# Kernel optimization log

Measured on AMD Instinct MI355X. Metric: run time of the kernel, lower is better.

## Reference

```python
import jax, jax.numpy as jnp
import numpy as np

HQ, HKV, HD = 16, 4, 64  # q heads, kv heads, head dim
ROPE_BASE = 10000.0


def _rope_tables(n, dim):
    inv_freq = 1.0 / (ROPE_BASE ** (jnp.arange(0, dim, 2, dtype=jnp.float32) / dim))
    t = jnp.arange(n, dtype=jnp.float32)
    freqs = jnp.outer(t, inv_freq)           # [N, dim/2]
    emb = jnp.concatenate([freqs, freqs], -1)  # [N, dim]
    return jnp.cos(emb), jnp.sin(emb)


def _rotate_half(x):
    h = x.shape[-1] // 2
    return jnp.concatenate([-x[..., h:], x[..., :h]], axis=-1)


def _apply_rope(x, cos, sin):
    # x: [B, N, H, D]; cos/sin: [N, D]
    c = cos[None, :, None, :]
    s = sin[None, :, None, :]
    return x * c + _rotate_half(x) * s


def setup_inputs() -> dict:
    key = jax.random.key(0)
    ks = jax.random.split(key, 5)
    B, N, D = 2, 4096, 1024
    kvD = HKV * HD
    sc = 0.02
    return {
        "x": jax.random.normal(ks[0], (B, N, D), jnp.float32),
        "Wq": jax.random.normal(ks[1], (D, D), jnp.float32) * sc,
        "Wk": jax.random.normal(ks[2], (D, kvD), jnp.float32) * sc,
        "Wv": jax.random.normal(ks[3], (D, kvD), jnp.float32) * sc,
        "Wo": jax.random.normal(ks[4], (D, D), jnp.float32) * sc,
    }


def reference(x, Wq, Wk, Wv, Wo):
    B, N, D = x.shape
    G = HQ // HKV
    Q = (x @ Wq).reshape(B, N, HQ, HD)
    K = (x @ Wk).reshape(B, N, HKV, HD)
    V = (x @ Wv).reshape(B, N, HKV, HD)

    cos, sin = _rope_tables(N, HD)
    Q = _apply_rope(Q, cos, sin)
    K = _apply_rope(K, cos, sin)

    # GQA: expand KV heads to match Q heads (repeat_interleave over head dim)
    K = jnp.repeat(K, G, axis=2)  # [B, N, HQ, HD]
    V = jnp.repeat(V, G, axis=2)

    Q = Q.transpose(0, 2, 1, 3)  # [B, HQ, N, HD]
    K = K.transpose(0, 2, 1, 3)
    V = V.transpose(0, 2, 1, 3)

    scores = jnp.einsum('bhqd,bhkd->bhqk', Q, K) / jnp.sqrt(jnp.float32(HD))
    attn = jax.nn.softmax(scores, axis=-1)
    out = jnp.einsum('bhqk,bhkd->bhqd', attn, V)  # [B, HQ, N, HD]
    out = out.transpose(0, 2, 1, 3).reshape(B, N, D)
    return out @ Wo
```

## Files before the change

kernel.cpp:

```cpp
#include <hip/hip_runtime.h>

#define HQn   16
#define HKVn  4
#define HDn   64
#define SEQN  4096
#define NB    2
#define DM    1024
#define KVD   256
#define NPACK 1536

#define QSCALE 0.18033688011112042f

typedef __attribute__((ext_vector_type(8))) short short8;
typedef __attribute__((ext_vector_type(4))) float f32x4;

#define MFMA16 __builtin_amdgcn_mfma_f32_16x16x32_bf16
#define EXP2F(x) __builtin_amdgcn_exp2f(x)

static __device__ __forceinline__ unsigned short f2bf(float f){
  union { float f; unsigned int u; } c; c.f = f;
  unsigned int r = c.u + 0x7fffu + ((c.u >> 16) & 1u);
  return (unsigned short)(r >> 16);
}

#if __has_builtin(__builtin_amdgcn_cvt_pk_bf16_f32)
typedef __attribute__((ext_vector_type(2))) __bf16 bf16x2v;
static __device__ __forceinline__ unsigned int pk_bf2(float a, float b){
  union { bf16x2v v; unsigned int u; } c;
  c.v = __builtin_amdgcn_cvt_pk_bf16_f32(a, b);
  return c.u;
}
#else
static __device__ __forceinline__ unsigned int pk_bf2(float a, float b){
  union { float f; unsigned int u; } ca, cb; ca.f = a; cb.f = b;
  return ((ca.u + 0x8000u) >> 16) | ((cb.u + 0x8000u) & 0xFFFF0000u);
}
#endif

static __device__ __forceinline__ void gl2lds16(const void* g, void* l){
  __builtin_amdgcn_global_load_lds(
      (const __attribute__((address_space(1))) void*)g,
      (__attribute__((address_space(3))) void*)l, 16, 0, 0);
}

__global__ __launch_bounds__(256) void prep_k(
    const float* __restrict__ x,
    const float* __restrict__ Wq, const float* __restrict__ Wk,
    const float* __restrict__ Wv, const float* __restrict__ Wo,
    float* __restrict__ ct, float* __restrict__ st,
    unsigned short* __restrict__ xb,
    unsigned short* __restrict__ Wqkv_t, unsigned short* __restrict__ Wot)
{
  const int id = blockIdx.x, tid = threadIdx.x;
  __shared__ float tile[64][65];

  if (id < 1024) {
    int idx = id * 256 + tid;
    int t = idx >> 6, d = idx & 63;
    int i = d & 31;
    float inv = 1.0f / powf(10000.0f, (float)i * (1.0f/32.0f));
    float ang = (float)t * inv;
    ct[t*HDn + d] = cosf(ang);
    st[t*HDn + d] = sinf(ang);
    return;
  }

  if (id < 5120) {
    size_t i = ((size_t)(id - 1024) * 256 + tid) * 8;
    float4 a = *(const float4*)(x + i);
    float4 b = *(const float4*)(x + i + 4);
    short8 o;
    o[0]=f2bf(a.x); o[1]=f2bf(a.y); o[2]=f2bf(a.z); o[3]=f2bf(a.w);
    o[4]=f2bf(b.x); o[5]=f2bf(b.y); o[6]=f2bf(b.z); o[7]=f2bf(b.w);
    *(short8*)(xb + i) = o;
    return;
  }

  const int cid = id - 5120;
  const int z = cid & 3;
  const int by = (cid >> 2) & 15;
  const int bx = cid >> 6;

  const float* W; unsigned short* D; int srcN, nOff;
  if      (z == 0) { W = Wq; D = Wqkv_t; srcN = DM;  nOff = 0;    }
  else if (z == 1) { W = Wo; D = Wot;    srcN = DM;  nOff = 0;    }
  else if (z == 2) { W = Wk; D = Wqkv_t; srcN = KVD; nOff = 1024; }
  else             { W = Wv; D = Wqkv_t; srcN = KVD; nOff = 1280; }
  const int n0 = by * 64;
  if (n0 >= srcN) return;
  const int k0 = bx * 64;

  const int lr = tid >> 4, lc = (tid & 15) * 4;
  #pragma unroll
  for (int p = 0; p < 4; p++) {
    float4 v = *(const float4*)&W[(size_t)(k0 + lr + p*16) * srcN + n0 + lc];
    tile[lr + p*16][lc+0] = v.x; tile[lr + p*16][lc+1] = v.y;
    tile[lr + p*16][lc+2] = v.z; tile[lr + p*16][lc+3] = v.w;
  }
  __syncthreads();

  const int nn = tid >> 2, kc = (tid & 3) * 16;
  unsigned short* dp = D + (size_t)(nOff + n0 + nn) * DM + k0 + kc;
  #pragma unroll
  for (int q = 0; q < 4; q++) {
    ushort4 o;
    o.x = f2bf(tile[kc + q*4 + 0][nn]);
    o.y = f2bf(tile[kc + q*4 + 1][nn]);
    o.z = f2bf(tile[kc + q*4 + 2][nn]);
    o.w = f2bf(tile[kc + q*4 + 3][nn]);
    *(ushort4*)(dp + q*4) = o;
  }
}

__global__ __launch_bounds__(256) void qkv2_k(
    const unsigned short* __restrict__ A, const unsigned short* __restrict__ Bt,
    const float* __restrict__ ct, const float* __restrict__ st,
    unsigned short* __restrict__ Qo, unsigned short* __restrict__ Ko,
    unsigned short* __restrict__ Vo)
{
  __shared__ __align__(16) short As[2][128][32];
  __shared__ __align__(16) short Bs[2][128][32];

  const int m0 = blockIdx.x * 128, n0 = blockIdx.y * 128;
  const int tid = threadIdx.x, lane = tid & 63, w = tid >> 6;
  const int wm = w >> 1, wn = w & 1;
  const int ln = lane & 15, quad = lane >> 4;

  f32x4 acc[4][4];
  #pragma unroll
  for (int i = 0; i < 4; i++)
    #pragma unroll
    for (int j = 0; j < 4; j++) acc[i][j] = (f32x4){0.f,0.f,0.f,0.f};

  const int r0 = tid >> 2, c8 = (tid & 3) * 8;
  const int r1 = r0 + 64;

  #define GSTAGE(cn, kk)                                                     \
    do {                                                                     \
      gl2lds16(A  + (size_t)(m0 + r0)*DM + (kk) + c8, &As[cn][r0][c8]);      \
      gl2lds16(A  + (size_t)(m0 + r1)*DM + (kk) + c8, &As[cn][r1][c8]);      \
      gl2lds16(Bt + (size_t)(n0 + r0)*DM + (kk) + c8, &Bs[cn][r0][c8]);      \
      gl2lds16(Bt + (size_t)(n0 + r1)*DM + (kk) + c8, &Bs[cn][r1][c8]);      \
    } while (0)

  GSTAGE(0, 0);
  __syncthreads();

  int cb = 0;
  for (int k0 = 0; k0 < DM; k0 += 32) {
    if (k0 + 32 < DM) GSTAGE(cb ^ 1, k0 + 32);

    short8 af[4], bf[4];
    #pragma unroll
    for (int mb = 0; mb < 4; mb++) af[mb] = *(const short8*)&As[cb][wm*64 + mb*16 + ln][quad*8];
    #pragma unroll
    for (int nb = 0; nb < 4; nb++) bf[nb] = *(const short8*)&Bs[cb][wn*64 + nb*16 + ln][quad*8];
    #pragma unroll
    for (int mb = 0; mb < 4; mb++)
      #pragma unroll
      for (int nb = 0; nb < 4; nb++)
        acc[mb][nb] = MFMA16(af[mb], bf[nb], acc[mb][nb], 0, 0, 0);

    __syncthreads();
    cb ^= 1;
  }
  #undef GSTAGE

  const int nc = n0 + wn*64;
  int kind, head;
  if (nc < 1024)      { kind = 0; head = nc >> 6;          }
  else if (nc < 1280) { kind = 1; head = (nc - 1024) >> 6; }
  else                { kind = 2; head = (nc - 1280) >> 6; }

  if (kind == 2) {
    #pragma unroll
    for (int mb = 0; mb < 4; mb++) {
      const int m = m0 + wm*64 + mb*16 + quad*4;
      const int t = m & (SEQN-1), b = m >> 12;
      #pragma unroll
      for (int nb = 0; nb < 4; nb++) {
        int d = nb*16 + ln;
        ushort4 pk;
        pk.x = f2bf(acc[mb][nb][0]); pk.y = f2bf(acc[mb][nb][1]);
        pk.z = f2bf(acc[mb][nb][2]); pk.w = f2bf(acc[mb][nb][3]);
        *(ushort4*)&Vo[(((size_t)(b*HKVn + head))*HDn + d)*SEQN + t] = pk;
      }
    }
  } else {
    #pragma unroll
    for (int mb = 0; mb < 4; mb++) {
      #pragma unroll
      for (int nb = 0; nb < 4; nb++) {
        #pragma unroll
        for (int r = 0; r < 4; r++) {
          int m = m0 + wm*64 + mb*16 + quad*4 + r;
          int t = m & (SEQN-1), b = m >> 12;
          int d = nb*16 + ln;
          float v = acc[mb][nb][r];
          float partner = (nb < 2) ? -acc[mb][nb+2][r] : acc[mb][nb-2][r];
          float cv = ct[t*HDn + d], sv = st[t*HDn + d];
          float o = v*cv + partner*sv;
          if (kind == 0) Qo[(((size_t)(b*HQn  + head))*SEQN + t)*HDn + d] = f2bf(o * QSCALE);
          else           Ko[(((size_t)(b*HKVn + head))*SEQN + t)*HDn + d] = f2bf(o);
        }
      }
    }
  }
}

__global__ __launch_bounds__(256, 4) void attn_k(
    const unsigned short* __restrict__ Q, const unsigned short* __restrict__ K,
    const unsigned short* __restrict__ Vt, unsigned short* __restrict__ AO)
{
  __shared__ __align__(16) short kb[2][64][64];
  __shared__ __align__(16) short vb[2][64][64];

  const int id  = blockIdx.x;
  const int bhv = id & 7;
  const int b   = bhv >> 2, hv = bhv & 3;
  const int rem = id >> 3;
  const int qt  = rem & 31;
  const int h   = hv*4 + (rem >> 5);
  const int q0  = qt * 128;

  const int tid = threadIdx.x, lane = tid & 63, w = tid >> 6;
  const int ln = lane & 15, quad = lane >> 4;

  const unsigned short* Qp = Q + (((size_t)(b*HQn + h))*SEQN + q0 + w*32) * HDn;
  const unsigned short* Kp = K + ((size_t)(b*HKVn + hv))*SEQN * HDn;
  const unsigned short* Vp = Vt + ((size_t)(b*HKVn + hv))*HDn * SEQN;

  short8 qf[2][2];
  qf[0][0] = *(const short8*)(Qp + ln*HDn + quad*8);
  qf[0][1] = *(const short8*)(Qp + ln*HDn + 32 + quad*8);
  qf[1][0] = *(const short8*)(Qp + (16+ln)*HDn + quad*8);
  qf[1][1] = *(const short8*)(Qp + (16+ln)*HDn + 32 + quad*8);

  short8 ones;
  #pragma unroll
  for (int j = 0; j < 8; j++) ones[j] = (short)0x3F80;

  f32x4 o[2][4], lacc[2];
  #pragma unroll
  for (int g = 0; g < 2; g++) {
    #pragma unroll
    for (int i = 0; i < 4; i++) o[g][i] = (f32x4){0.f,0.f,0.f,0.f};
    lacc[g] = (f32x4){0.f,0.f,0.f,0.f};
  }

  const int w2   = w & 1;
  const int lrow = lane >> 3;
  const int slin = lane & 7;
  const int sK   = slin ^ lrow;

  int kkey[4]; size_t vrow[4];
  #pragma unroll
  for (int i = 0; i < 4; i++) {
    kkey[i] = 32*w2 + 16*(i & 1) + 8*(lrow >> 2) + 4*(i >> 1) + (lrow & 3);
    vrow[i] = (size_t)(w2*32 + i*8 + lrow) * SEQN;
  }

  #define STAGE(cn, kts)                                                     \
    do {                                                                     \
      if (w < 2) {                                                           \
        _Pragma("unroll")                                                    \
        for (int i = 0; i < 4; i++)                                          \
          gl2lds16(Kp + (size_t)((kts) + kkey[i])*HDn + sK*8,                \
                   &kb[cn][w2*32 + i*8][0]);                                 \
      } else {                                                               \
        _Pragma("unroll")                                                    \
        for (int i = 0; i < 4; i++)                                          \
          gl2lds16(Vp + vrow[i] + (kts) + sK*8,                              \
                   &vb[cn][w2*32 + i*8][0]);                                 \
      }                                                                      \
    } while (0)

  const int swz0 = (( quad      ^ (ln & 7)) * 8);
  const int swz1 = (((quad + 4) ^ (ln & 7)) * 8);

  STAGE(0, 0);
  __syncthreads();

  int c = 0;
  for (int kt = 0; kt < SEQN; kt += 64) {
    if (kt + 64 < SEQN) STAGE(c ^ 1, kt + 64);

    f32x4 s[2][4];
    __builtin_amdgcn_s_setprio(1);
    #pragma unroll
    for (int nb = 0; nb < 4; nb++) {
      short8 k0 = *(const short8*)&kb[c][nb*16 + ln][swz0];
      short8 k1 = *(const short8*)&kb[c][nb*16 + ln][swz1];
      f32x4 t0 = (f32x4){0.f,0.f,0.f,0.f};
      t0 = MFMA16(k0, qf[0][0], t0, 0, 0, 0);
      t0 = MFMA16(k1, qf[0][1], t0, 0, 0, 0);
      s[0][nb] = t0;
      f32x4 t1 = (f32x4){0.f,0.f,0.f,0.f};
      t1 = MFMA16(k0, qf[1][0], t1, 0, 0, 0);
      t1 = MFMA16(k1, qf[1][1], t1, 0, 0, 0);
      s[1][nb] = t1;
    }
    __builtin_amdgcn_s_setprio(0);

    short8 pf[2][2];
    #pragma unroll
    for (int g = 0; g < 2; g++) {
      #pragma unroll
      for (int k2 = 0; k2 < 2; k2++) {
        union { short8 s8; unsigned u[4]; } f;
        f.u[0] = pk_bf2(EXP2F(s[g][2*k2  ][0]), EXP2F(s[g][2*k2  ][1]));
        f.u[1] = pk_bf2(EXP2F(s[g][2*k2  ][2]), EXP2F(s[g][2*k2  ][3]));
        f.u[2] = pk_bf2(EXP2F(s[g][2*k2+1][0]), EXP2F(s[g][2*k2+1][1]));
        f.u[3] = pk_bf2(EXP2F(s[g][2*k2+1][2]), EXP2F(s[g][2*k2+1][3]));
        pf[g][k2] = f.s8;
      }
    }

    __builtin_amdgcn_s_setprio(1);
    #pragma unroll
    for (int db = 0; db < 4; db++) {
      short8 v0 = *(const short8*)&vb[c][db*16 + ln][swz0];
      short8 v1 = *(const short8*)&vb[c][db*16 + ln][swz1];
      o[0][db] = MFMA16(pf[0][0], v0, o[0][db], 0, 0, 0);
      o[0][db] = MFMA16(pf[0][1], v1, o[0][db], 0, 0, 0);
      o[1][db] = MFMA16(pf[1][0], v0, o[1][db], 0, 0, 0);
      o[1][db] = MFMA16(pf[1][1], v1, o[1][db], 0, 0, 0);
    }
    lacc[0] = MFMA16(pf[0][0], ones, lacc[0], 0, 0, 0);
    lacc[0] = MFMA16(pf[0][1], ones, lacc[0], 0, 0, 0);
    lacc[1] = MFMA16(pf[1][0], ones, lacc[1], 0, 0, 0);
    lacc[1] = MFMA16(pf[1][1], ones, lacc[1], 0, 0, 0);
    __builtin_amdgcn_s_setprio(0);

    __syncthreads();
    c ^= 1;
  }
  #undef STAGE

  #pragma unroll
  for (int g = 0; g < 2; g++) {
    float inv[4];
    #pragma unroll
    for (int r = 0; r < 4; r++) inv[r] = 1.0f / lacc[g][r];
    #pragma unroll
    for (int db = 0; db < 4; db++) {
      #pragma unroll
      for (int r = 0; r < 4; r++) {
        int gq = q0 + w*32 + g*16 + quad*4 + r;
        int d  = db*16 + ln;
        AO[(((size_t)(b*SEQN + gq))*HQn + h)*HDn + d] = f2bf(o[g][db][r] * inv[r]);
      }
    }
  }
}

__global__ __launch_bounds__(256) void oproj2_k(
    const unsigned short* __restrict__ A, const unsigned short* __restrict__ Bt,
    float* __restrict__ out)
{
  __shared__ __align__(16) short As[2][128][32];
  __shared__ __align__(16) short Bs[2][128][32];

  const int m0 = blockIdx.x * 128, n0 = blockIdx.y * 128;
  const int tid = threadIdx.x, lane = tid & 63, w = tid >> 6;
  const int wm = w >> 1, wn = w & 1;
  const int ln = lane & 15, quad = lane >> 4;

  f32x4 acc[4][4];
  #pragma unroll
  for (int i = 0; i < 4; i++)
    #pragma unroll
    for (int j = 0; j < 4; j++) acc[i][j] = (f32x4){0.f,0.f,0.f,0.f};

  const int r0 = tid >> 2, c8 = (tid & 3) * 8;
  const int r1 = r0 + 64;

  #define GSTAGE(cn, kk)                                                     \
    do {                                                                     \
      gl2lds16(A  + (size_t)(m0 + r0)*DM + (kk) + c8, &As[cn][r0][c8]);      \
      gl2lds16(A  + (size_t)(m0 + r1)*DM + (kk) + c8, &As[cn][r1][c8]);      \
      gl2lds16(Bt + (size_t)(n0 + r0)*DM + (kk) + c8, &Bs[cn][r0][c8]);      \
      gl2lds16(Bt + (size_t)(n0 + r1)*DM + (kk) + c8, &Bs[cn][r1][c8]);      \
    } while (0)

  GSTAGE(0, 0);
  __syncthreads();

  int cb = 0;
  for (int k0 = 0; k0 < DM; k0 += 32) {
    if (k0 + 32 < DM) GSTAGE(cb ^ 1, k0 + 32);

    short8 af[4], bf[4];
    #pragma unroll
    for (int mb = 0; mb < 4; mb++) af[mb] = *(const short8*)&As[cb][wm*64 + mb*16 + ln][quad*8];
    #pragma unroll
    for (int nb = 0; nb < 4; nb++) bf[nb] = *(const short8*)&Bs[cb][wn*64 + nb*16 + ln][quad*8];
    #pragma unroll
    for (int mb = 0; mb < 4; mb++)
      #pragma unroll
      for (int nb = 0; nb < 4; nb++)
        acc[mb][nb] = MFMA16(af[mb], bf[nb], acc[mb][nb], 0, 0, 0);

    __syncthreads();
    cb ^= 1;
  }
  #undef GSTAGE

  #pragma unroll
  for (int mb = 0; mb < 4; mb++) {
    #pragma unroll
    for (int nb = 0; nb < 4; nb++) {
      #pragma unroll
      for (int r = 0; r < 4; r++) {
        int m = m0 + wm*64 + mb*16 + quad*4 + r;
        int c = n0 + wn*64 + nb*16 + ln;
        out[(size_t)m*DM + c] = acc[mb][nb][r];
      }
    }
  }
}

extern "C" void kernel_launch(void* const* d_in, const int* in_sizes, int n_in,
                              void* d_out, int out_size, void* d_ws, size_t ws_size,
                              hipStream_t stream) {
  const float* x  = (const float*)d_in[0];
  const float* Wq = (const float*)d_in[1];
  const float* Wk = (const float*)d_in[2];
  const float* Wv = (const float*)d_in[3];
  const float* Wo = (const float*)d_in[4];
  float* out = (float*)d_out;

  char* ws = (char*)d_ws;
  float* cos_t = (float*)ws;
  float* sin_t = cos_t + SEQN*HDn;
  unsigned short* xb     = (unsigned short*)(sin_t + SEQN*HDn);
  unsigned short* AO     = xb;
  unsigned short* Wqkv_t = xb + (size_t)NB*SEQN*DM;
  unsigned short* Wot    = Wqkv_t + (size_t)NPACK*DM;
  unsigned short* Qb     = Wot + (size_t)DM*DM;
  unsigned short* Kb     = Qb + (size_t)NB*HQn *SEQN*HDn;
  unsigned short* Vb     = Kb + (size_t)NB*HKVn*SEQN*HDn;

  hipLaunchKernelGGL(prep_k, dim3(6144), dim3(256), 0, stream,
                     x, Wq, Wk, Wv, Wo, cos_t, sin_t, xb, Wqkv_t, Wot);
  hipLaunchKernelGGL(qkv2_k, dim3(64, 12), dim3(256), 0, stream,
                     xb, Wqkv_t, cos_t, sin_t, Qb, Kb, Vb);
  hipLaunchKernelGGL(attn_k, dim3(1024), dim3(256), 0, stream,
                     Qb, Kb, Vb, AO);
  hipLaunchKernelGGL(oproj2_k, dim3(64, 8), dim3(256), 0, stream,
                     AO, Wot, out);
}
```

Measured before the change: 290.2 us.

## Software-pipeline attention loop: defer PV MFMA one tile behind QK

Restructures the attention inner loop so the P·V matrix multiplies for the previous key tile are issued right after the current tile's QK^T multiplies, overlapping the exp/pack work with MFMA execution. V buffers become triple-buffered in LDS to keep the previous tile's V alive, and a final PV step drains the pipeline after the loop. Occupancy is pinned via waves_per_eu(4,4) instead of launch_bounds min blocks. This adds LDS usage and carries pf across iterations, which raises register pressure.

```diff
diff --git a/kernel.cpp b/kernel.cpp
--- a/kernel.cpp
+++ b/kernel.cpp
@@ -208,12 +208,13 @@
   }
 }
 
-__global__ __launch_bounds__(256, 4) void attn_k(
+__global__ __launch_bounds__(256) __attribute__((amdgpu_waves_per_eu(4, 4)))
+void attn_k(
     const unsigned short* __restrict__ Q, const unsigned short* __restrict__ K,
     const unsigned short* __restrict__ Vt, unsigned short* __restrict__ AO)
 {
   __shared__ __align__(16) short kb[2][64][64];
-  __shared__ __align__(16) short vb[2][64][64];
+  __shared__ __align__(16) short vb[3][64][64];
 
   const int id  = blockIdx.x;
   const int bhv = id & 7;
@@ -260,37 +261,56 @@
     vrow[i] = (size_t)(w2*32 + i*8 + lrow) * SEQN;
   }
 
-  #define STAGE(cn, kts)                                                     \
+  #define STAGE(kcn, vcn, kts)                                               \
     do {                                                                     \
       if (w < 2) {                                                           \
         _Pragma("unroll")                                                    \
         for (int i = 0; i < 4; i++)                                          \
           gl2lds16(Kp + (size_t)((kts) + kkey[i])*HDn + sK*8,                \
-                   &kb[cn][w2*32 + i*8][0]);                                 \
+                   &kb[kcn][w2*32 + i*8][0]);                                \
       } else {                                                               \
         _Pragma("unroll")                                                    \
         for (int i = 0; i < 4; i++)                                          \
           gl2lds16(Vp + vrow[i] + (kts) + sK*8,                              \
-                   &vb[cn][w2*32 + i*8][0]);                                 \
+                   &vb[vcn][w2*32 + i*8][0]);                                \
       }                                                                      \
     } while (0)
 
+  #define PVSTEP(slot)                                                       \
+    do {                                                                     \
+      _Pragma("unroll")                                                      \
+      for (int db = 0; db < 4; db++) {                                       \
+        short8 v0 = *(const short8*)&vb[slot][db*16 + ln][swz0];             \
+        short8 v1 = *(const short8*)&vb[slot][db*16 + ln][swz1];             \
+        o[0][db] = MFMA16(pf[0][0], v0, o[0][db], 0, 0, 0);                  \
+        o[0][db] = MFMA16(pf[0][1], v1, o[0][db], 0, 0, 0);                  \
+        o[1][db] = MFMA16(pf[1][0], v0, o[1][db], 0, 0, 0);                  \
+        o[1][db] = MFMA16(pf[1][1], v1, o[1][db], 0, 0, 0);                  \
+      }                                                                      \
+      lacc[0] = MFMA16(pf[0][0], ones, lacc[0], 0, 0, 0);                    \
+      lacc[0] = MFMA16(pf[0][1], ones, lacc[0], 0, 0, 0);                    \
+      lacc[1] = MFMA16(pf[1][0], ones, lacc[1], 0, 0, 0);                    \
+      lacc[1] = MFMA16(pf[1][1], ones, lacc[1], 0, 0, 0);                    \
+    } while (0)
+
   const int swz0 = (( quad      ^ (ln & 7)) * 8);
   const int swz1 = (((quad + 4) ^ (ln & 7)) * 8);
 
-  STAGE(0, 0);
+  STAGE(0, 0, 0);
   __syncthreads();
 
-  int c = 0;
+  short8 pf[2][2];
+  int kc = 0, vprev = 2, vcur = 0, vnext = 1;
+
   for (int kt = 0; kt < SEQN; kt += 64) {
-    if (kt + 64 < SEQN) STAGE(c ^ 1, kt + 64);
-
+    if (kt + 64 < SEQN) STAGE(kc ^ 1, vnext, kt + 64);
+
+    __builtin_amdgcn_s_setprio(1);
     f32x4 s[2][4];
-    __builtin_amdgcn_s_setprio(1);
     #pragma unroll
     for (int nb = 0; nb < 4; nb++) {
-      short8 k0 = *(const short8*)&kb[c][nb*16 + ln][swz0];
-      short8 k1 = *(const short8*)&kb[c][nb*16 + ln][swz1];
+      short8 k0 = *(const short8*)&kb[kc][nb*16 + ln][swz0];
+      short8 k1 = *(const short8*)&kb[kc][nb*16 + ln][swz1];
       f32x4 t0 = (f32x4){0.f,0.f,0.f,0.f};
       t0 = MFMA16(k0, qf[0][0], t0, 0, 0, 0);
       t0 = MFMA16(k1, qf[0][1], t0, 0, 0, 0);
@@ -300,9 +320,10 @@
       t1 = MFMA16(k1, qf[1][1], t1, 0, 0, 0);
       s[1][nb] = t1;
     }
+
+    if (kt) PVSTEP(vprev);
     __builtin_amdgcn_s_setprio(0);
 
-    short8 pf[2][2];
     #pragma unroll
     for (int g = 0; g < 2; g++) {
       #pragma unroll
@@ -316,25 +337,15 @@
       }
     }
 
-    __builtin_amdgcn_s_setprio(1);
-    #pragma unroll
-    for (int db = 0; db < 4; db++) {
-      short8 v0 = *(const short8*)&vb[c][db*16 + ln][swz0];
-      short8 v1 = *(const short8*)&vb[c][db*16 + ln][swz1];
-      o[0][db] = MFMA16(pf[0][0], v0, o[0][db], 0, 0, 0);
-      o[0][db] = MFMA16(pf[0][1], v1, o[0][db], 0, 0, 0);
-      o[1][db] = MFMA16(pf[1][0], v0, o[1][db], 0, 0, 0);
-      o[1][db] = MFMA16(pf[1][1], v1, o[1][db], 0, 0, 0);
-    }
-    lacc[0] = MFMA16(pf[0][0], ones, lacc[0], 0, 0, 0);
-    lacc[0] = MFMA16(pf[0][1], ones, lacc[0], 0, 0, 0);
-    lacc[1] = MFMA16(pf[1][0], ones, lacc[1], 0, 0, 0);
-    lacc[1] = MFMA16(pf[1][1], ones, lacc[1], 0, 0, 0);
-    __builtin_amdgcn_s_setprio(0);
-
     __syncthreads();
-    c ^= 1;
-  }
+    kc ^= 1;
+    int tmp = vprev; vprev = vcur; vcur = vnext; vnext = tmp;
+  }
+
+  __builtin_amdgcn_s_setprio(1);
+  PVSTEP(vprev);
+  __builtin_amdgcn_s_setprio(0);
+  #undef PVSTEP
   #undef STAGE
 
   #pragma unroll
```

New measurement: 323.5 us. 11.5% more time.
